# Optimization experiments

Hardware: AMD Instinct MI355X
Metric: run time of the kernel (lower is better)

The kernel has to match this reference:

```python
import jax, jax.numpy as jnp
import numpy as np

D_STATE = 8
DT_RANK = 16
D_CONV = 4


def layernorm(x, w, b, eps=1e-5):
    mu = jnp.mean(x, axis=-1, keepdims=True)
    var = jnp.var(x, axis=-1, keepdims=True)
    return (x - mu) * jax.lax.rsqrt(var + eps) * w + b


def silu(x):
    return x * jax.nn.sigmoid(x)


def dwconv_causal(x, w, b):
    # x: [B,L,D], w: [D,K] depthwise causal conv (mamba conv1d, padding=K-1 then truncate)
    K = w.shape[1]
    xp = jnp.pad(x, ((0, 0), (K - 1, 0), (0, 0)))
    y = jax.lax.conv_general_dilated(
        xp, w.T[:, None, :], (1,), 'VALID',
        dimension_numbers=('NWC', 'WIO', 'NWC'),
        feature_group_count=w.shape[0])
    return y + b


def selective_scan(u, dt, A, Bm, Cm, Dp):
    # u, dt: [b,l,d]; A: [d,n]; Bm, Cm: [b,l,n]; Dp: [d]
    def step(h, inp):
        dt_t, B_t, C_t, u_t = inp           # [b,d],[b,n],[b,n],[b,d]
        dA = jnp.exp(dt_t[..., None] * A)   # [b,d,n]
        h = dA * h + dt_t[..., None] * B_t[:, None, :] * u_t[..., None]
        y = jnp.einsum('bdn,bn->bd', h, C_t)
        return h, y
    b, l, d = u.shape
    h0 = jnp.zeros((b, d, A.shape[1]), u.dtype)
    xs = (dt.transpose(1, 0, 2), Bm.transpose(1, 0, 2),
          Cm.transpose(1, 0, 2), u.transpose(1, 0, 2))
    _, ys = jax.lax.scan(step, h0, xs)
    return ys.transpose(1, 0, 2) + u * Dp


def scan_dir(x, xe, cw, cb, cew, ceb, xpw, dtw, dtb, A_log, Dp):
    # one scan direction: u from x (input0 path), dt/B/C from xe (extra_emb path)
    xc = silu(dwconv_causal(x, cw, cb))
    ec = silu(dwconv_causal(xe, cew, ceb))
    dbl = ec @ xpw.T                                   # [b,l,dt_rank+2n]
    dtr = dbl[..., :DT_RANK]
    Bm = dbl[..., DT_RANK:DT_RANK + D_STATE]
    Cm = dbl[..., DT_RANK + D_STATE:]
    dt = jax.nn.softplus(dtr @ dtw.T + dtb)
    A = -jnp.exp(A_log)
    return selective_scan(xc, dt, A, Bm, Cm, Dp)


def forward(input0, input1, norm0_w, norm0_b, norm1_w, norm1_b,
            in_proj_w, in_proj_extra_w,
            convx_w, convx_b, conve_w, conve_b,
            convx_w_r, convx_b_r, conve_w_r, conve_b_r,
            xproj_w, xproj_w_r, dtproj_w, dtproj_b, dtproj_w_r, dtproj_b_r,
            A_log, A_log_r, Dp, Dp_r, outnorm_w, outnorm_b, outproj_w):
    skip = input0
    h0 = layernorm(input0, norm0_w, norm0_b)
    h1 = layernorm(input1, norm1_w, norm1_b)
    xz = h0 @ in_proj_w.T                     # [b,l,2d]
    d = in_proj_w.shape[0] // 2
    x, z = xz[..., :d], xz[..., d:]
    xe = h1 @ in_proj_extra_w.T               # [b,l,d]
    # forward-direction scan
    y_f = scan_dir(x, xe, convx_w, convx_b, conve_w, conve_b,
                   xproj_w, dtproj_w, dtproj_b, A_log, Dp)
    # backward-direction scan (flip sequence, scan, flip back)
    xr, xer = jnp.flip(x, 1), jnp.flip(xe, 1)
    y_b = scan_dir(xr, xer, convx_w_r, convx_b_r, conve_w_r, conve_b_r,
                   xproj_w_r, dtproj_w_r, dtproj_b_r, A_log_r, Dp_r)
    y = (y_f + jnp.flip(y_b, 1)) * 0.5        # if_devide_out=True
    y = layernorm(y, outnorm_w, outnorm_b)    # use_norm=True
    y = y * silu(z)
    out = y @ outproj_w.T
    return out + skip


def setup_inputs() -> dict:
    key = jax.random.key(0)
    B, H, W, dim = 2, 128, 128, 256
    L, d, n, dtr, K = H * W, dim, D_STATE, DT_RANK, D_CONV
    ks = jax.random.split(key, 24)
    s = 0.02
    inp = {
        'input0': jax.random.normal(ks[0], (B, L, dim), jnp.float32),
        'input1': jax.random.normal(ks[1], (B, L, dim), jnp.float32),
        'norm0_w': jnp.ones((dim,), jnp.float32),
        'norm0_b': jnp.zeros((dim,), jnp.float32),
        'norm1_w': jnp.ones((dim,), jnp.float32),
        'norm1_b': jnp.zeros((dim,), jnp.float32),
        'in_proj_w': jax.random.normal(ks[2], (2 * d, dim), jnp.float32) * s,
        'in_proj_extra_w': jax.random.normal(ks[3], (d, dim), jnp.float32) * s,
        'convx_w': jax.random.normal(ks[4], (d, K), jnp.float32) * 0.2,
        'convx_b': jnp.zeros((d,), jnp.float32),
        'conve_w': jax.random.normal(ks[5], (d, K), jnp.float32) * 0.2,
        'conve_b': jnp.zeros((d,), jnp.float32),
        'convx_w_r': jax.random.normal(ks[6], (d, K), jnp.float32) * 0.2,
        'convx_b_r': jnp.zeros((d,), jnp.float32),
        'conve_w_r': jax.random.normal(ks[7], (d, K), jnp.float32) * 0.2,
        'conve_b_r': jnp.zeros((d,), jnp.float32),
        'xproj_w': jax.random.normal(ks[8], (dtr + 2 * n, d), jnp.float32) * s,
        'xproj_w_r': jax.random.normal(ks[9], (dtr + 2 * n, d), jnp.float32) * s,
        'dtproj_w': jax.random.normal(ks[10], (d, dtr), jnp.float32) * 0.1,
        'dtproj_b': jax.random.uniform(ks[11], (d,), jnp.float32, -4.0, -2.0),
        'dtproj_w_r': jax.random.normal(ks[12], (d, dtr), jnp.float32) * 0.1,
        'dtproj_b_r': jax.random.uniform(ks[13], (d,), jnp.float32, -4.0, -2.0),
        'A_log': jnp.tile(jnp.log(jnp.arange(1, n + 1, dtype=jnp.float32)), (d, 1)),
        'A_log_r': jnp.tile(jnp.log(jnp.arange(1, n + 1, dtype=jnp.float32)), (d, 1)),
        'Dp': jnp.ones((d,), jnp.float32),
        'Dp_r': jnp.ones((d,), jnp.float32),
        'outnorm_w': jnp.ones((d,), jnp.float32),
        'outnorm_b': jnp.zeros((d,), jnp.float32),
        'outproj_w': jax.random.normal(ks[14], (dim, d), jnp.float32) * s,
    }
    return inp


def reference(input0, input1, norm0_w, norm0_b, norm1_w, norm1_b,
              in_proj_w, in_proj_extra_w,
              convx_w, convx_b, conve_w, conve_b,
              convx_w_r, convx_b_r, conve_w_r, conve_b_r,
              xproj_w, xproj_w_r, dtproj_w, dtproj_b, dtproj_w_r, dtproj_b_r,
              A_log, A_log_r, Dp, Dp_r, outnorm_w, outnorm_b, outproj_w):
    return forward(input0, input1, norm0_w, norm0_b, norm1_w, norm1_b,
                   in_proj_w, in_proj_extra_w,
                   convx_w, convx_b, conve_w, conve_b,
                   convx_w_r, convx_b_r, conve_w_r, conve_b_r,
                   xproj_w, xproj_w_r, dtproj_w, dtproj_b, dtproj_w_r, dtproj_b_r,
                   A_log, A_log_r, Dp, Dp_r, outnorm_w, outnorm_b, outproj_w)
```

## Files before the change

kernel.cpp:

```cpp
#include <hip/hip_runtime.h>
#include <math.h>

#define L_SEQ 16384
#define DIM 256
#define NST 8
#define RNK 16
#define S_TOT 32768
#define NCH 512
#define CLH 32

typedef __attribute__((ext_vector_type(8))) short bf16x8;
typedef __attribute__((ext_vector_type(4))) float f32x4;

__device__ __forceinline__ float bf2f(unsigned short u) {
  union { unsigned int i; float f; } v; v.i = ((unsigned int)u) << 16; return v.f;
}
__device__ __forceinline__ unsigned short f2bf(float x) {
  union { float f; unsigned int i; } v; v.f = x;
  unsigned int r = v.i + 0x7fffu + ((v.i >> 16) & 1u);
  return (unsigned short)(r >> 16);
}
__device__ __forceinline__ float rcpf(float x) {
  return __builtin_amdgcn_rcpf(x);
}

__global__ __launch_bounds__(256) void ln_norm(
    const float* __restrict__ in0, const float* __restrict__ in1,
    const float* __restrict__ w0, const float* __restrict__ b0,
    const float* __restrict__ w1, const float* __restrict__ b1,
    unsigned short* __restrict__ h0, unsigned short* __restrict__ h1,
    const float* __restrict__ pw0, const float* __restrict__ pw1,
    const float* __restrict__ pw2, unsigned short* __restrict__ wbout) {
  int which = blockIdx.y;
  if (which == 0 && blockIdx.x < 1024) {
    int i = blockIdx.x * 256 + threadIdx.x;
    if (i < 131072) wbout[i] = f2bf(pw0[i]);
    else if (i < 196608) wbout[i] = f2bf(pw1[i - 131072]);
    else wbout[i] = f2bf(pw2[i - 196608]);
  }
  int row = blockIdx.x * 4 + (threadIdx.x >> 6);
  int lane = threadIdx.x & 63;
  const float* x = (which ? in1 : in0) + (size_t)row * DIM;
  const float* w = which ? w1 : w0;
  const float* b = which ? b1 : b0;
  unsigned short* h = which ? h1 : h0;
  float4 v = *(const float4*)&x[lane * 4];
  float s = v.x + v.y + v.z + v.w;
  float s2 = v.x * v.x + v.y * v.y + v.z * v.z + v.w * v.w;
  for (int off = 32; off; off >>= 1) {
    s += __shfl_xor(s, off);
    s2 += __shfl_xor(s2, off);
  }
  float mean = s * (1.0f / DIM);
  float var = s2 * (1.0f / DIM) - mean * mean;
  float rstd = rsqrtf(var + 1e-5f);
  float4 wv = *(const float4*)&w[lane * 4];
  float4 bv = *(const float4*)&b[lane * 4];
  ushort4 out;
  out.x = f2bf((v.x - mean) * rstd * wv.x + bv.x);
  out.y = f2bf((v.y - mean) * rstd * wv.y + bv.y);
  out.z = f2bf((v.z - mean) * rstd * wv.z + bv.z);
  out.w = f2bf((v.w - mean) * rstd * wv.w + bv.w);
  *(ushort4*)&h[(size_t)row * DIM + lane * 4] = out;
}

template <int BF16C, int ADDIN>
__global__ __launch_bounds__(256) void gemm64(
    const unsigned short* __restrict__ A, int lda,
    const unsigned short* __restrict__ Wb,
    void* __restrict__ Cv, const float* __restrict__ addp, int Nn) {
  __shared__ unsigned short As[64 * 256];
  __shared__ unsigned short Ws[64 * 256];
  int tid = threadIdx.x;
  int n0 = blockIdx.x * 64, m0 = blockIdx.y * 64;
  for (int i = 0; i < 8; ++i) {
    int f8 = tid + i * 256;
    int r = f8 >> 5, c8 = (f8 & 31) * 8;
    int sc = c8 ^ ((r & 7) << 3);
    *(uint4*)&As[r * 256 + sc] = *(const uint4*)&A[(size_t)(m0 + r) * lda + c8];
    *(uint4*)&Ws[r * 256 + sc] = *(const uint4*)&Wb[(size_t)(n0 + r) * 256 + c8];
  }
  __syncthreads();
  int wid = tid >> 6, lane = tid & 63;
  int wm = wid >> 1, wn = wid & 1;
  int l15 = lane & 15, lk = (lane >> 4) * 8;
  f32x4 acc[2][2] = {};
  for (int ks = 0; ks < 8; ++ks) {
    int kcol = ks * 32 + lk;
    bf16x8 af[2], bf_[2];
    for (int mf = 0; mf < 2; ++mf) {
      int row = wm * 32 + mf * 16 + l15;
      af[mf] = *(const bf16x8*)&As[row * 256 + (kcol ^ ((row & 7) << 3))];
    }
    for (int nf = 0; nf < 2; ++nf) {
      int row = wn * 32 + nf * 16 + l15;
      bf_[nf] = *(const bf16x8*)&Ws[row * 256 + (kcol ^ ((row & 7) << 3))];
    }
    for (int mf = 0; mf < 2; ++mf)
      for (int nf = 0; nf < 2; ++nf)
        acc[mf][nf] = __builtin_amdgcn_mfma_f32_16x16x32_bf16(
            af[mf], bf_[nf], acc[mf][nf], 0, 0, 0);
  }
  for (int mf = 0; mf < 2; ++mf)
    for (int nf = 0; nf < 2; ++nf) {
      int row = m0 + wm * 32 + mf * 16 + (lane >> 4) * 4;
      int col = n0 + wn * 32 + nf * 16 + l15;
      for (int v = 0; v < 4; ++v) {
        size_t off = (size_t)(row + v) * Nn + col;
        float val = acc[mf][nf][v];
        if (ADDIN) val += addp[off];
        if (BF16C) ((unsigned short*)Cv)[off] = f2bf(val);
        else       ((float*)Cv)[off] = val;
      }
    }
}

__global__ __launch_bounds__(256) void xproj_mfma(
    const unsigned short* __restrict__ xe,
    const float* __restrict__ conve_w, const float* __restrict__ conve_b,
    const float* __restrict__ conve_w_r, const float* __restrict__ conve_b_r,
    const float* __restrict__ xproj_w, const float* __restrict__ xproj_w_r,
    unsigned short* __restrict__ dbl2) {
  __shared__ unsigned short ecS[64 * 256];
  __shared__ unsigned short xwS[32 * 256];
  int chunk = blockIdx.x;
  int dir = blockIdx.y;
  int b = chunk >> 8;
  int t0 = (chunk & 255) * 64;
  int tid = threadIdx.x;
  const float* cw = dir ? conve_w_r : conve_w;
  const float* cb = dir ? conve_b_r : conve_b;
  const float* xw = dir ? xproj_w_r : xproj_w;

  for (int i = tid; i < 32 * 256; i += 256) {
    int o = i >> 8, dd = i & 255;
    xwS[o * 256 + (((dd & ~7) ^ ((o & 7) << 3)) | (dd & 7))] = f2bf(xw[i]);
  }

  {
    int c = tid;
    float w0 = cw[c * 4 + 0], w1 = cw[c * 4 + 1], w2 = cw[c * 4 + 2],
          w3 = cw[c * 4 + 3], bias = cb[c];
    size_t bL = (size_t)b * L_SEQ;
    auto loadx = [&](int t) -> float {
      if (t < 0) return 0.f;
      int src = dir ? (L_SEQ - 1 - t) : t;
      return bf2f(xe[(bL + src) * DIM + c]);
    };
    float xm3 = loadx(t0 - 3), xm2 = loadx(t0 - 2), xm1 = loadx(t0 - 1);
    const unsigned short* xp =
        &xe[(bL + (dir ? (L_SEQ - 1 - t0) : t0)) * DIM + c];
    int xstep = dir ? -DIM : DIM;
    int cbase = c & ~7, clow = c & 7;
    for (int t4 = 0; t4 < 64; t4 += 4) {
      float xin4[4];
      for (int j = 0; j < 4; ++j) xin4[j] = bf2f(xp[(ptrdiff_t)j * xstep]);
      xp += (ptrdiff_t)4 * xstep;
      for (int j = 0; j < 4; ++j) {
        int tl = t4 + j;
        float xin = xin4[j];
        float pre = w0 * xm3 + w1 * xm2 + w2 * xm1 + w3 * xin + bias;
        float u = pre * rcpf(1.f + __expf(-pre));
        xm3 = xm2; xm2 = xm1; xm1 = xin;
        ecS[tl * 256 + ((cbase ^ ((tl & 7) << 3)) | clow)] = f2bf(u);
      }
    }
  }
  __syncthreads();

  int wid = tid >> 6, lane = tid & 63;
  int l15 = lane & 15, lk = (lane >> 4) * 8;
  f32x4 acc[2] = {};
  for (int kk = 0; kk < 8; ++kk) {
    int kcol = kk * 32 + lk;
    int row = wid * 16 + l15;
    bf16x8 af = *(const bf16x8*)&ecS[row * 256 + (kcol ^ ((row & 7) << 3))];
    for (int ni = 0; ni < 2; ++ni) {
      int o = ni * 16 + l15;
      bf16x8 bfr = *(const bf16x8*)&xwS[o * 256 + (kcol ^ ((o & 7) << 3))];
      acc[ni] = __builtin_amdgcn_mfma_f32_16x16x32_bf16(af, bfr, acc[ni], 0, 0, 0);
    }
  }
  size_t mbase = (size_t)dir * S_TOT + (size_t)chunk * 64;
  int rloc = wid * 16 + (lane >> 4) * 4;
  for (int ni = 0; ni < 2; ++ni) {
    int o = ni * 16 + l15;
    for (int v = 0; v < 4; ++v)
      dbl2[(mbase + rloc + v) * 32 + o] = f2bf(acc[ni][v]);
  }
}

__global__ __launch_bounds__(256) void dtu_compute(
    const unsigned short* __restrict__ dbl2,
    const float* __restrict__ dtw, const float* __restrict__ dtw_r,
    const float* __restrict__ dtb, const float* __restrict__ dtb_r,
    unsigned short* __restrict__ dt_arr,
    const unsigned short* __restrict__ xz,
    const float* __restrict__ convx_w, const float* __restrict__ convx_b,
    const float* __restrict__ convx_w_r, const float* __restrict__ convx_b_r,
    unsigned short* __restrict__ u_arr) {
  __shared__ unsigned short dtwS[256 * 32];
  __shared__ unsigned short dtrS[64 * 32];
  __shared__ unsigned short outS[64 * 256];
  int tid = threadIdx.x;
  if (blockIdx.x < 1024) {
    int m0 = blockIdx.x * 64;
    int dir = (blockIdx.x >= 512) ? 1 : 0;
    const float* dw = dir ? dtw_r : dtw;
    const float* db = dir ? dtb_r : dtb;
    {
      uint4 z; z.x = 0; z.y = 0; z.z = 0; z.w = 0;
      for (int i = tid; i < 1280; i += 256) {
        if (i < 1024) ((uint4*)dtwS)[i] = z;
        else          ((uint4*)dtrS)[i - 1024] = z;
      }
    }
    __syncthreads();
    for (int it = 0; it < 4; ++it) {
      int idx = tid + it * 256;
      int c = idx >> 2, k4 = idx & 3;
      float4 v = *(const float4*)&dw[c * 16 + k4 * 4];
      uint2 pk;
      pk.x = (unsigned int)f2bf(v.x) | ((unsigned int)f2bf(v.y) << 16);
      pk.y = (unsigned int)f2bf(v.z) | ((unsigned int)f2bf(v.w) << 16);
      int byte = c * 64 + (((k4 >> 1) ^ (c & 3)) << 4) + ((k4 & 1) << 3);
      *(uint2*)((char*)dtwS + byte) = pk;
    }
    {
      int r = tid >> 2, k4 = tid & 3;
      uint2 pk = *(const uint2*)&dbl2[(size_t)(m0 + r) * 32 + k4 * 4];
      int byte = r * 64 + (((k4 >> 1) ^ (r & 3)) << 4) + ((k4 & 1) << 3);
      *(uint2*)((char*)dtrS + byte) = pk;
    }
    __syncthreads();
    int wid = tid >> 6, lane = tid & 63;
    int l15 = lane & 15, lkc = lane >> 4;
    bf16x8 af[4];
    for (int mi = 0; mi < 4; ++mi) {
      int r = mi * 16 + l15;
      af[mi] = *(const bf16x8*)((char*)dtrS + r * 64 + ((lkc ^ (r & 3)) << 4));
    }
    f32x4 acc[4][4] = {};
    for (int ni = 0; ni < 4; ++ni) {
      int c = (wid * 4 + ni) * 16 + l15;
      bf16x8 bfr = *(const bf16x8*)((char*)dtwS + c * 64 + ((lkc ^ (c & 3)) << 4));
      for (int mi = 0; mi < 4; ++mi)
        acc[mi][ni] = __builtin_amdgcn_mfma_f32_16x16x32_bf16(
            af[mi], bfr, acc[mi][ni], 0, 0, 0);
    }
    for (int ni = 0; ni < 4; ++ni) {
      int c = (wid * 4 + ni) * 16 + l15;
      float bias_ = db[c];
      int cb_ = c & ~7, cl_ = c & 7;
      for (int mi = 0; mi < 4; ++mi) {
        int rb = mi * 16 + (lane >> 4) * 4;
        for (int v = 0; v < 4; ++v) {
          int r = rb + v;
          float xdt = acc[mi][ni][v] + bias_;
          float dtv = (xdt > 15.f) ? xdt : __logf(1.f + __expf(xdt));
          outS[r * 256 + ((cb_ ^ ((r & 7) << 3)) | cl_)] = f2bf(dtv);
        }
      }
    }
    __syncthreads();
    for (int it = 0; it < 8; ++it) {
      int i = tid + it * 256;
      int r = i >> 5, cg = (i & 31) * 8;
      uint4 val = *(const uint4*)&outS[r * 256 + (cg ^ ((r & 7) << 3))];
      *(uint4*)&dt_arr[(size_t)(m0 + r) * 256 + cg] = val;
    }
  } else {
    int chunk = blockIdx.x - 1024;
    int b = chunk >> 9;
    int t0 = (chunk & 511) * 32;
    int c = tid;
    float w0 = convx_w[c * 4 + 0], w1 = convx_w[c * 4 + 1],
          w2 = convx_w[c * 4 + 2], w3 = convx_w[c * 4 + 3], bias = convx_b[c];
    float w0r = convx_w_r[c * 4 + 0], w1r = convx_w_r[c * 4 + 1],
          w2r = convx_w_r[c * 4 + 2], w3r = convx_w_r[c * 4 + 3],
          biasr = convx_b_r[c];
    size_t bL = (size_t)b * L_SEQ;
    auto ld = [&](int t) -> float {
      if (t < 0 || t >= L_SEQ) return 0.f;
      return bf2f(xz[(bL + t) * 512 + c]);
    };
    float x3 = ld(t0 - 3), x2 = ld(t0 - 2), x1 = ld(t0 - 1);
    unsigned short* op0 = &u_arr[(bL + t0) * DIM + c];
    unsigned short* op1 =
        &u_arr[((size_t)S_TOT + bL + (L_SEQ - 1 - t0)) * DIM + c];
    for (int tg = 0; tg < 36; tg += 4) {
      float xin4[4];
      for (int j = 0; j < 4; ++j) xin4[j] = ld(t0 + tg + j);
      for (int j = 0; j < 4; ++j) {
        int tl = tg + j;
        float xin = xin4[j];
        if (tl < 32) {
          float pre = w0 * x3 + w1 * x2 + w2 * x1 + w3 * xin + bias;
          op0[(size_t)tl * DIM] = f2bf(pre * rcpf(1.f + __expf(-pre)));
        }
        if (tl >= 3 && tl < 35) {
          float prer = w0r * xin + w1r * x1 + w2r * x2 + w3r * x3 + biasr;
          int s = tl - 3;
          *(op1 - (ptrdiff_t)s * DIM) = f2bf(prer * rcpf(1.f + __expf(-prer)));
        }
        x3 = x2; x2 = x1; x1 = xin;
      }
    }
  }
}

#define DA8(FASTA)                                                    \
  float dA[NST];                                                      \
  if (FASTA) {                                                        \
    float e1 = __expf(-dtv);                                          \
    dA[0] = e1;                                                       \
    for (int n = 1; n < NST; ++n) dA[n] = dA[n - 1] * e1;             \
  } else {                                                            \
    for (int n = 0; n < NST; ++n) dA[n] = __expf(dtv * Ar[n]);        \
  }

template <int USE_UDT>
__global__ __launch_bounds__(256) void scan_pass1(
    const unsigned short* __restrict__ xz, const unsigned short* __restrict__ dbl2,
    const unsigned short* __restrict__ u_arr,
    const unsigned short* __restrict__ dt_arr,
    const float* __restrict__ convx_w, const float* __restrict__ convx_b,
    const float* __restrict__ convx_w_r, const float* __restrict__ convx_b_r,
    const float* __restrict__ dtproj_w, const float* __restrict__ dtproj_b,
    const float* __restrict__ dtproj_w_r, const float* __restrict__ dtproj_b_r,
    const float* __restrict__ A_log, const float* __restrict__ A_log_r,
    float* __restrict__ Pc, float* __restrict__ Qc) {
  int chunk = blockIdx.x, b = blockIdx.y, dir = blockIdx.z;
  int d = threadIdx.x;
  const float* al = dir ? A_log_r : A_log;
  float w0 = 0.f, w1 = 0.f, w2 = 0.f, w3 = 0.f, bias = 0.f, dbias = 0.f;
  float dwreg[RNK];
  if (!USE_UDT) {
    const float* cw = dir ? convx_w_r : convx_w;
    const float* cb = dir ? convx_b_r : convx_b;
    const float* dw = dir ? dtproj_w_r : dtproj_w;
    const float* dbp = dir ? dtproj_b_r : dtproj_b;
    w0 = cw[d * 4 + 0]; w1 = cw[d * 4 + 1]; w2 = cw[d * 4 + 2];
    w3 = cw[d * 4 + 3]; bias = cb[d]; dbias = dbp[d];
    for (int r = 0; r < RNK; ++r) dwreg[r] = dw[d * RNK + r];
  }
  float Ar[NST];
  bool fa = true;
  for (int n = 0; n < NST; ++n) {
    Ar[n] = -__expf(al[d * NST + n]);
    fa = fa && (fabsf(Ar[n] + (float)(n + 1)) < 1e-4f * (float)(n + 1));
  }
  bool fastA = (__ballot(fa) == ~0ULL);

  __shared__ float dblS[CLH][32];
  int t0 = chunk * CLH;
  size_t dtbase = (size_t)dir * S_TOT + (size_t)b * L_SEQ;
  if (USE_UDT) {
    int i = d;
    dblS[i >> 3][i & 7] =
        bf2f(dbl2[(dtbase + t0 + (i >> 3)) * 32 + 16 + (i & 7)]);
  } else {
    for (int i = d; i < CLH * 32; i += 256)
      dblS[i >> 5][i & 31] = bf2f(dbl2[(dtbase + t0) * 32 + i]);
  }
  __syncthreads();
  auto loadx = [&](int t) -> float {
    if (t < 0) return 0.f;
    int srct = dir ? (L_SEQ - 1 - t) : t;
    return bf2f(xz[((size_t)b * L_SEQ + srct) * 512 + d]);
  };
  float xm3 = 0.f, xm2 = 0.f, xm1 = 0.f;
  if (!USE_UDT) { xm3 = loadx(t0 - 3); xm2 = loadx(t0 - 2); xm1 = loadx(t0 - 1); }
  const unsigned short* up = &u_arr[(dtbase + t0) * DIM + d];
  const unsigned short* dtp = &dt_arr[(dtbase + t0) * DIM + d];
  float Q[NST];
  for (int n = 0; n < NST; ++n) Q[n] = 0.f;
  float sdt = 0.f;
  const int BOFF = USE_UDT ? 0 : 16;

#define P1_GRP(FASTA)                                                      \
  for (int t8 = 0; t8 < CLH; t8 += 8) {                                    \
    float uu[8], dd[8];                                                    \
    for (int j = 0; j < 8; ++j) {                                          \
      uu[j] = bf2f(up[(size_t)j * DIM]);                                   \
      dd[j] = bf2f(dtp[(size_t)j * DIM]);                                  \
    }                                                                      \
    up += 8 * DIM; dtp += 8 * DIM;                                         \
    for (int j = 0; j < 8; ++j) {                                          \
      const float* row = dblS[t8 + j];                                     \
      float u = uu[j], dtv = dd[j];                                        \
      float du = dtv * u;                                                  \
      sdt += dtv;                                                          \
      DA8(FASTA)                                                           \
      float4 B0 = *(const float4*)(row);                                   \
      float4 B1 = *(const float4*)(row + 4);                               \
      Q[0] = dA[0] * Q[0] + du * B0.x; Q[1] = dA[1] * Q[1] + du * B0.y;    \
      Q[2] = dA[2] * Q[2] + du * B0.z; Q[3] = dA[3] * Q[3] + du * B0.w;    \
      Q[4] = dA[4] * Q[4] + du * B1.x; Q[5] = dA[5] * Q[5] + du * B1.y;    \
      Q[6] = dA[6] * Q[6] + du * B1.z; Q[7] = dA[7] * Q[7] + du * B1.w;    \
    }                                                                      \
  }

#define P1_STEP(FASTA)                                                     \
  {                                                                        \
    const float* row = dblS[tl];                                           \
    float u, dtv;                                                          \
    {                                                                      \
      float xin = loadx(t0 + tl);                                          \
      float pre = w0 * xm3 + w1 * xm2 + w2 * xm1 + w3 * xin + bias;        \
      u = pre * rcpf(1.f + __expf(-pre));                                  \
      xm3 = xm2; xm2 = xm1; xm1 = xin;                                     \
      float4 q0 = *(const float4*)(row);                                   \
      float4 q1 = *(const float4*)(row + 4);                               \
      float4 q2 = *(const float4*)(row + 8);                               \
      float4 q3 = *(const float4*)(row + 12);                              \
      float xdt = dbias + q0.x * dwreg[0] + q0.y * dwreg[1] +              \
                  q0.z * dwreg[2] + q0.w * dwreg[3] + q1.x * dwreg[4] +    \
                  q1.y * dwreg[5] + q1.z * dwreg[6] + q1.w * dwreg[7] +    \
                  q2.x * dwreg[8] + q2.y * dwreg[9] + q2.z * dwreg[10] +   \
                  q2.w * dwreg[11] + q3.x * dwreg[12] + q3.y * dwreg[13] + \
                  q3.z * dwreg[14] + q3.w * dwreg[15];                     \
      dtv = (xdt > 15.f) ? xdt : __logf(1.f + __expf(xdt));                \
    }                                                                      \
    float du = dtv * u;                                                    \
    sdt += dtv;                                                            \
    DA8(FASTA)                                                             \
    float4 B0 = *(const float4*)(row + BOFF);                              \
    float4 B1 = *(const float4*)(row + BOFF + 4);                          \
    Q[0] = dA[0] * Q[0] + du * B0.x; Q[1] = dA[1] * Q[1] + du * B0.y;      \
    Q[2] = dA[2] * Q[2] + du * B0.z; Q[3] = dA[3] * Q[3] + du * B0.w;      \
    Q[4] = dA[4] * Q[4] + du * B1.x; Q[5] = dA[5] * Q[5] + du * B1.y;      \
    Q[6] = dA[6] * Q[6] + du * B1.z; Q[7] = dA[7] * Q[7] + du * B1.w;      \
  }

  if (USE_UDT) {
    if (fastA) { P1_GRP(1) } else { P1_GRP(0) }
  } else {
    if (fastA) {
      for (int tl = 0; tl < CLH; ++tl) P1_STEP(1)
    } else {
      for (int tl = 0; tl < CLH; ++tl) P1_STEP(0)
    }
  }
#undef P1_STEP
#undef P1_GRP

  float P[NST];
  if (fastA) {
    float E = __expf(-sdt);
    P[0] = E;
    for (int n = 1; n < NST; ++n) P[n] = P[n - 1] * E;
  } else {
    for (int n = 0; n < NST; ++n) P[n] = __expf(Ar[n] * sdt);
  }
  size_t obase = ((((size_t)(dir * 2 + b)) * NCH + chunk) * DIM + d) * NST;
  for (int n = 0; n < NST; ++n) { Pc[obase + n] = P[n]; Qc[obase + n] = Q[n]; }
}

__global__ __launch_bounds__(256) void scan_mid(
    float* __restrict__ Pc, const float* __restrict__ Qc) {
  int idx = blockIdx.x * 256 + threadIdx.x;
  int dn = idx & 2047;
  int db_ = idx >> 11;
  size_t base = (size_t)db_ * NCH * 2048 + dn;
  float h = 0.f;
  for (int c0 = 0; c0 < NCH; c0 += 8) {
    size_t off = base + (size_t)c0 * 2048;
    float P[8], Q[8];
#pragma unroll
    for (int j = 0; j < 8; ++j) {
      P[j] = Pc[off + (size_t)j * 2048];
      Q[j] = Qc[off + (size_t)j * 2048];
    }
#pragma unroll
    for (int j = 0; j < 8; ++j) {
      Pc[off + (size_t)j * 2048] = h;
      h = P[j] * h + Q[j];
    }
  }
}

template <int MODE>
__global__ __launch_bounds__(256) void scan_pass2(
    const unsigned short* __restrict__ xz, const unsigned short* __restrict__ dbl2,
    unsigned short* __restrict__ u_arr,
    const unsigned short* __restrict__ dt_arr,
    const float* __restrict__ convx_w, const float* __restrict__ convx_b,
    const float* __restrict__ convx_w_r, const float* __restrict__ convx_b_r,
    const float* __restrict__ dtproj_w, const float* __restrict__ dtproj_b,
    const float* __restrict__ dtproj_w_r, const float* __restrict__ dtproj_b_r,
    const float* __restrict__ A_log, const float* __restrict__ A_log_r,
    const float* __restrict__ Dp, const float* __restrict__ Dp_r,
    const float* __restrict__ Hinit, unsigned short* __restrict__ ycomb,
    int dirParam) {
  int chunk = blockIdx.x, b = blockIdx.y;
  int dir = MODE ? blockIdx.z : dirParam;
  int d = threadIdx.x;
  const float* al = dir ? A_log_r : A_log;
  float Dv = (dir ? Dp_r : Dp)[d];
  float w0 = 0.f, w1 = 0.f, w2 = 0.f, w3 = 0.f, bias = 0.f, dbias = 0.f;
  float dwreg[RNK];
  if (!MODE) {
    const float* cw = dir ? convx_w_r : convx_w;
    const float* cb = dir ? convx_b_r : convx_b;
    const float* dw = dir ? dtproj_w_r : dtproj_w;
    const float* dbp = dir ? dtproj_b_r : dtproj_b;
    w0 = cw[d * 4 + 0]; w1 = cw[d * 4 + 1]; w2 = cw[d * 4 + 2];
    w3 = cw[d * 4 + 3]; bias = cb[d];
    dbias = dbp[d];
    for (int r = 0; r < RNK; ++r) dwreg[r] = dw[d * RNK + r];
  }
  float Ar[NST];
  bool fa = true;
  for (int n = 0; n < NST; ++n) {
    Ar[n] = -__expf(al[d * NST + n]);
    fa = fa && (fabsf(Ar[n] + (float)(n + 1)) < 1e-4f * (float)(n + 1));
  }
  bool fastA = (__ballot(fa) == ~0ULL);

  __shared__ float dblS[CLH][32];
  int t0 = chunk * CLH;
  size_t dtbase = (size_t)dir * S_TOT + (size_t)b * L_SEQ;
  if (MODE) {
    for (int i = d; i < CLH * 16; i += 256)
      dblS[i >> 4][i & 15] =
          bf2f(dbl2[(dtbase + t0 + (i >> 4)) * 32 + 16 + (i & 15)]);
  } else {
    for (int i = d; i < CLH * 32; i += 256)
      dblS[i >> 5][i & 31] = bf2f(dbl2[(dtbase + t0) * 32 + i]);
  }
  __syncthreads();
  auto loadx = [&](int t) -> float {
    if (t < 0) return 0.f;
    int srct = dir ? (L_SEQ - 1 - t) : t;
    return bf2f(xz[((size_t)b * L_SEQ + srct) * 512 + d]);
  };
  float xm3 = 0.f, xm2 = 0.f, xm1 = 0.f;
  if (!MODE) { xm3 = loadx(t0 - 3); xm2 = loadx(t0 - 2); xm1 = loadx(t0 - 1); }
  float h[NST];
  size_t hbase = ((((size_t)(dir * 2 + b)) * NCH + chunk) * DIM + d) * NST;
  for (int n = 0; n < NST; ++n) h[n] = Hinit[hbase + n];
  unsigned short* up = &u_arr[(dtbase + t0) * DIM + d];
  const unsigned short* dtp = &dt_arr[(dtbase + t0) * DIM + d];
  unsigned short* yc = &ycomb[((size_t)b * L_SEQ + t0) * DIM + d];

#define P2_GRP(FASTA)                                                      \
  for (int t8 = 0; t8 < CLH; t8 += 8) {                                    \
    float uu[8], dd[8];                                                    \
    for (int j = 0; j < 8; ++j) {                                          \
      uu[j] = bf2f(up[(size_t)j * DIM]);                                   \
      dd[j] = bf2f(dtp[(size_t)j * DIM]);                                  \
    }                                                                      \
    for (int j = 0; j < 8; ++j) {                                          \
      const float* row = dblS[t8 + j];                                     \
      float u = uu[j], dtv = dd[j];                                        \
      float du = dtv * u;                                                  \
      DA8(FASTA)                                                           \
      float4 B0 = *(const float4*)(row);                                   \
      float4 B1 = *(const float4*)(row + 4);                               \
      float4 C0 = *(const float4*)(row + 8);                               \
      float4 C1 = *(const float4*)(row + 12);                              \
      h[0] = dA[0] * h[0] + du * B0.x; h[1] = dA[1] * h[1] + du * B0.y;    \
      h[2] = dA[2] * h[2] + du * B0.z; h[3] = dA[3] * h[3] + du * B0.w;    \
      h[4] = dA[4] * h[4] + du * B1.x; h[5] = dA[5] * h[5] + du * B1.y;    \
      h[6] = dA[6] * h[6] + du * B1.z; h[7] = dA[7] * h[7] + du * B1.w;    \
      float y = C0.x * h[0] + C0.y * h[1] + C0.z * h[2] + C0.w * h[3] +    \
                C1.x * h[4] + C1.y * h[5] + C1.z * h[6] + C1.w * h[7] +    \
                u * Dv;                                                    \
      if (dir == 0) yc[(size_t)j * DIM] = f2bf(y);                         \
      else          up[(size_t)j * DIM] = f2bf(y);                         \
    }                                                                      \
    up += 8 * DIM; dtp += 8 * DIM; yc += 8 * DIM;                          \
  }

#define P2_STEP(FASTA)                                                     \
  {                                                                        \
    int t = t0 + tl;                                                       \
    const float* row = dblS[tl];                                           \
    float u, dtv;                                                          \
    {                                                                      \
      float xin = loadx(t);                                                \
      float pre = w0 * xm3 + w1 * xm2 + w2 * xm1 + w3 * xin + bias;        \
      u = pre * rcpf(1.f + __expf(-pre));                                  \
      xm3 = xm2; xm2 = xm1; xm1 = xin;                                     \
      float4 q0 = *(const float4*)(row);                                   \
      float4 q1 = *(const float4*)(row + 4);                               \
      float4 q2 = *(const float4*)(row + 8);                               \
      float4 q3 = *(const float4*)(row + 12);                              \
      float xdt = dbias + q0.x * dwreg[0] + q0.y * dwreg[1] +              \
                  q0.z * dwreg[2] + q0.w * dwreg[3] + q1.x * dwreg[4] +    \
                  q1.y * dwreg[5] + q1.z * dwreg[6] + q1.w * dwreg[7] +    \
                  q2.x * dwreg[8] + q2.y * dwreg[9] + q2.z * dwreg[10] +   \
                  q2.w * dwreg[11] + q3.x * dwreg[12] + q3.y * dwreg[13] + \
                  q3.z * dwreg[14] + q3.w * dwreg[15];                     \
      dtv = (xdt > 15.f) ? xdt : __logf(1.f + __expf(xdt));                \
    }                                                                      \
    float du = dtv * u;                                                    \
    DA8(FASTA)                                                             \
    float4 B0 = *(const float4*)(row + 16);                                \
    float4 B1 = *(const float4*)(row + 20);                                \
    float4 C0 = *(const float4*)(row + 24);                                \
    float4 C1 = *(const float4*)(row + 28);                                \
    h[0] = dA[0] * h[0] + du * B0.x; h[1] = dA[1] * h[1] + du * B0.y;      \
    h[2] = dA[2] * h[2] + du * B0.z; h[3] = dA[3] * h[3] + du * B0.w;      \
    h[4] = dA[4] * h[4] + du * B1.x; h[5] = dA[5] * h[5] + du * B1.y;      \
    h[6] = dA[6] * h[6] + du * B1.z; h[7] = dA[7] * h[7] + du * B1.w;      \
    float y = C0.x * h[0] + C0.y * h[1] + C0.z * h[2] + C0.w * h[3] +      \
              C1.x * h[4] + C1.y * h[5] + C1.z * h[6] + C1.w * h[7] +      \
              u * Dv;                                                      \
    if (dir == 0) {                                                        \
      ycomb[((size_t)b * L_SEQ + t) * DIM + d] = f2bf(y);                  \
    } else {                                                               \
      size_t o = ((size_t)b * L_SEQ + (L_SEQ - 1 - t)) * DIM + d;          \
      float prev = bf2f(ycomb[o]);                                         \
      ycomb[o] = f2bf(0.5f * (prev + y));                                  \
    }                                                                      \
  }

  if (MODE) {
    if (fastA) { P2_GRP(1) } else { P2_GRP(0) }
  } else {
    if (fastA) {
      for (int tl = 0; tl < CLH; ++tl) P2_STEP(1)
    } else {
      for (int tl = 0; tl < CLH; ++tl) P2_STEP(0)
    }
  }
#undef P2_STEP
#undef P2_GRP
}

template <int MERGED>
__global__ __launch_bounds__(256) void combine_ln(
    const unsigned short* __restrict__ ycomb,
    const unsigned short* __restrict__ ybu,
    unsigned short* __restrict__ xz,
    const float* __restrict__ onw, const float* __restrict__ onb) {
  int m = blockIdx.x * 4 + (threadIdx.x >> 6);
  int lane = threadIdx.x & 63;
  ushort4 y4 = *(const ushort4*)&ycomb[(size_t)m * DIM + lane * 4];
  float v0 = bf2f(y4.x), v1 = bf2f(y4.y), v2 = bf2f(y4.z), v3 = bf2f(y4.w);
  if (MERGED) {
    int b = m >> 14, l = m & (L_SEQ - 1);
    size_t fo = ((size_t)S_TOT + (size_t)b * L_SEQ + (L_SEQ - 1 - l)) * DIM +
                lane * 4;
    ushort4 yb4 = *(const ushort4*)&ybu[fo];
    v0 = 0.5f * (v0 + bf2f(yb4.x)); v1 = 0.5f * (v1 + bf2f(yb4.y));
    v2 = 0.5f * (v2 + bf2f(yb4.z)); v3 = 0.5f * (v3 + bf2f(yb4.w));
  }
  float s = v0 + v1 + v2 + v3;
  float s2 = v0 * v0 + v1 * v1 + v2 * v2 + v3 * v3;
  for (int off = 32; off; off >>= 1) {
    s += __shfl_xor(s, off);
    s2 += __shfl_xor(s2, off);
  }
  float mean = s * (1.0f / DIM);
  float var = s2 * (1.0f / DIM) - mean * mean;
  float rstd = rsqrtf(var + 1e-5f);
  ushort4 z4 = *(const ushort4*)&xz[(size_t)m * 512 + 256 + lane * 4];
  float zf[4] = {bf2f(z4.x), bf2f(z4.y), bf2f(z4.z), bf2f(z4.w)};
  float vf[4] = {v0, v1, v2, v3};
  ushort4 out;
  unsigned short* op = (unsigned short*)&out;
  for (int j = 0; j < 4; ++j) {
    int c = lane * 4 + j;
    float ln = (vf[j] - mean) * rstd * onw[c] + onb[c];
    op[j] = f2bf(ln * (zf[j] * rcpf(1.f + __expf(-zf[j]))));
  }
  *(ushort4*)&xz[(size_t)m * 512 + lane * 4] = out;
}

extern "C" void kernel_launch(void* const* d_in, const int* in_sizes, int n_in,
                              void* d_out, int out_size, void* d_ws, size_t ws_size,
                              hipStream_t stream) {
  const float* input0 = (const float*)d_in[0];
  const float* input1 = (const float*)d_in[1];
  const float* norm0_w = (const float*)d_in[2];
  const float* norm0_b = (const float*)d_in[3];
  const float* norm1_w = (const float*)d_in[4];
  const float* norm1_b = (const float*)d_in[5];
  const float* in_proj_w = (const float*)d_in[6];
  const float* in_proj_extra_w = (const float*)d_in[7];
  const float* convx_w = (const float*)d_in[8];
  const float* convx_b = (const float*)d_in[9];
  const float* conve_w = (const float*)d_in[10];
  const float* conve_b = (const float*)d_in[11];
  const float* convx_w_r = (const float*)d_in[12];
  const float* convx_b_r = (const float*)d_in[13];
  const float* conve_w_r = (const float*)d_in[14];
  const float* conve_b_r = (const float*)d_in[15];
  const float* xproj_w = (const float*)d_in[16];
  const float* xproj_w_r = (const float*)d_in[17];
  const float* dtproj_w = (const float*)d_in[18];
  const float* dtproj_b = (const float*)d_in[19];
  const float* dtproj_w_r = (const float*)d_in[20];
  const float* dtproj_b_r = (const float*)d_in[21];
  const float* A_log = (const float*)d_in[22];
  const float* A_log_r = (const float*)d_in[23];
  const float* Dp = (const float*)d_in[24];
  const float* Dp_r = (const float*)d_in[25];
  const float* outnorm_w = (const float*)d_in[26];
  const float* outnorm_b = (const float*)d_in[27];
  const float* outproj_w = (const float*)d_in[28];

  char* w = (char*)d_ws;
  unsigned short* xz    = (unsigned short*)(w + 0);
  unsigned short* h1    = (unsigned short*)(w + 0);
  unsigned short* h0    = (unsigned short*)(w + 33554432);
  unsigned short* ycomb = (unsigned short*)(w + 33554432);
  float* Qc   = (float*)(w + 33554432);
  unsigned short* xe    = (unsigned short*)(w + 50331648);
  float* Pc   = (float*)(w + 50331648);
  unsigned short* dbl2 = (unsigned short*)(w + 67108864);
  unsigned short* wb = (unsigned short*)(w + 75497472);
  unsigned short* wb_in  = wb;
  unsigned short* wb_ex  = wb + 131072;
  unsigned short* wb_out = wb + 196608;
  unsigned short* u_arr  = (unsigned short*)(w + 76021760);
  unsigned short* dt_arr = (unsigned short*)(w + 109576192);
  const bool big = ws_size >= 76021760ULL + 67108864ULL;

  ln_norm<<<dim3(S_TOT / 4, 2), 256, 0, stream>>>(
      input0, input1, norm0_w, norm0_b, norm1_w, norm1_b, h0, h1,
      in_proj_w, in_proj_extra_w, outproj_w, wb);
  gemm64<1, 0><<<dim3(4, 512), 256, 0, stream>>>(h1, DIM, wb_ex, xe, nullptr, 256);
  gemm64<1, 0><<<dim3(8, 512), 256, 0, stream>>>(h0, DIM, wb_in, xz, nullptr, 512);
  xproj_mfma<<<dim3(512, 2), 256, 0, stream>>>(
      xe, conve_w, conve_b, conve_w_r, conve_b_r, xproj_w, xproj_w_r, dbl2);
  if (big) {
    dtu_compute<<<dim3(2048), 256, 0, stream>>>(
        dbl2, dtproj_w, dtproj_w_r, dtproj_b, dtproj_b_r, dt_arr,
        xz, convx_w, convx_b, convx_w_r, convx_b_r, u_arr);
    scan_pass1<1><<<dim3(NCH, 2, 2), 256, 0, stream>>>(
        xz, dbl2, u_arr, dt_arr, convx_w, convx_b, convx_w_r, convx_b_r,
        dtproj_w, dtproj_b, dtproj_w_r, dtproj_b_r, A_log, A_log_r, Pc, Qc);
  } else {
    scan_pass1<0><<<dim3(NCH, 2, 2), 256, 0, stream>>>(
        xz, dbl2, u_arr, dt_arr, convx_w, convx_b, convx_w_r, convx_b_r,
        dtproj_w, dtproj_b, dtproj_w_r, dtproj_b_r, A_log, A_log_r, Pc, Qc);
  }
  scan_mid<<<dim3(32), 256, 0, stream>>>(Pc, Qc);
  if (big) {
    scan_pass2<1><<<dim3(NCH, 2, 2), 256, 0, stream>>>(
        xz, dbl2, u_arr, dt_arr, convx_w, convx_b, convx_w_r, convx_b_r,
        dtproj_w, dtproj_b, dtproj_w_r, dtproj_b_r, A_log, A_log_r,
        Dp, Dp_r, Pc, ycomb, 0);
    combine_ln<1><<<dim3(S_TOT / 4), 256, 0, stream>>>(
        ycomb, u_arr, xz, outnorm_w, outnorm_b);
  } else {
    for (int dir = 0; dir < 2; ++dir)
      scan_pass2<0><<<dim3(NCH, 2), 256, 0, stream>>>(
          xz, dbl2, u_arr, dt_arr, convx_w, convx_b, convx_w_r, convx_b_r,
          dtproj_w, dtproj_b, dtproj_w_r, dtproj_b_r, A_log, A_log_r,
          Dp, Dp_r, Pc, ycomb, dir);
    combine_ln<0><<<dim3(S_TOT / 4), 256, 0, stream>>>(
        ycomb, nullptr, xz, outnorm_w, outnorm_b);
  }
  gemm64<0, 1><<<dim3(4, 512), 256, 0, stream>>>(
      xz, 512, wb_out, d_out, input0, 256);
}
```

Measured before the change: 219.0 us.

## Merge input GEMMs into one launch and fuse combine+layernorm+gate into output GEMM

The two input projection GEMMs now run as one grid that selects its operand by block index, with h1 moved to a separate buffer so both can run together. The forward/backward combine, output layernorm and SiLU gate are folded into the A-tile load of the output projection GEMM. This removes a launch and the bf16 round trip of the gated activations through xz, at the cost of redoing the layernorm per N-tile (4x redundant loads and math) and more LDS traffic.

Measured after the change: 237.8 us. +8.6%, slower.

```diff
diff --git a/kernel.cpp b/kernel.cpp
--- a/kernel.cpp
+++ b/kernel.cpp
@@ -111,6 +111,182 @@
         if (ADDIN) val += addp[off];
         if (BF16C) ((unsigned short*)Cv)[off] = f2bf(val);
         else       ((float*)Cv)[off] = val;
+      }
+    }
+}
+
+__global__ __launch_bounds__(256) void gemm_in(
+    const unsigned short* __restrict__ h0, const unsigned short* __restrict__ h1,
+    const unsigned short* __restrict__ wb_in, const unsigned short* __restrict__ wb_ex,
+    unsigned short* __restrict__ xzOut, unsigned short* __restrict__ xeOut) {
+  __shared__ unsigned short As[64 * 256];
+  __shared__ unsigned short Ws[64 * 256];
+  int tid = threadIdx.x;
+  bool isX = blockIdx.x >= 4;
+  const unsigned short* A = isX ? h0 : h1;
+  const unsigned short* Wb = isX ? wb_in : wb_ex;
+  unsigned short* Cv = isX ? xzOut : xeOut;
+  int Nn = isX ? 512 : 256;
+  int n0 = (isX ? (int)blockIdx.x - 4 : (int)blockIdx.x) * 64;
+  int m0 = blockIdx.y * 64;
+  for (int i = 0; i < 8; ++i) {
+    int f8 = tid + i * 256;
+    int r = f8 >> 5, c8 = (f8 & 31) * 8;
+    int sc = c8 ^ ((r & 7) << 3);
+    *(uint4*)&As[r * 256 + sc] = *(const uint4*)&A[(size_t)(m0 + r) * 256 + c8];
+    *(uint4*)&Ws[r * 256 + sc] = *(const uint4*)&Wb[(size_t)(n0 + r) * 256 + c8];
+  }
+  __syncthreads();
+  int wid = tid >> 6, lane = tid & 63;
+  int wm = wid >> 1, wn = wid & 1;
+  int l15 = lane & 15, lk = (lane >> 4) * 8;
+  f32x4 acc[2][2] = {};
+  for (int ks = 0; ks < 8; ++ks) {
+    int kcol = ks * 32 + lk;
+    bf16x8 af[2], bf_[2];
+    for (int mf = 0; mf < 2; ++mf) {
+      int row = wm * 32 + mf * 16 + l15;
+      af[mf] = *(const bf16x8*)&As[row * 256 + (kcol ^ ((row & 7) << 3))];
+    }
+    for (int nf = 0; nf < 2; ++nf) {
+      int row = wn * 32 + nf * 16 + l15;
+      bf_[nf] = *(const bf16x8*)&Ws[row * 256 + (kcol ^ ((row & 7) << 3))];
+    }
+    for (int mf = 0; mf < 2; ++mf)
+      for (int nf = 0; nf < 2; ++nf)
+        acc[mf][nf] = __builtin_amdgcn_mfma_f32_16x16x32_bf16(
+            af[mf], bf_[nf], acc[mf][nf], 0, 0, 0);
+  }
+  for (int mf = 0; mf < 2; ++mf)
+    for (int nf = 0; nf < 2; ++nf) {
+      int row = m0 + wm * 32 + mf * 16 + (lane >> 4) * 4;
+      int col = n0 + wn * 32 + nf * 16 + l15;
+      for (int v = 0; v < 4; ++v) {
+        size_t off = (size_t)(row + v) * Nn + col;
+        Cv[off] = f2bf(acc[mf][nf][v]);
+      }
+    }
+}
+
+__global__ __launch_bounds__(256) void gemm_out_fused(
+    const unsigned short* __restrict__ ycomb,
+    const unsigned short* __restrict__ ybu,
+    const unsigned short* __restrict__ xz,
+    const float* __restrict__ onw, const float* __restrict__ onb,
+    const unsigned short* __restrict__ Wb,
+    float* __restrict__ outp, const float* __restrict__ addp) {
+  __shared__ unsigned short As[64 * 256];
+  __shared__ unsigned short Ws[64 * 256];
+  __shared__ float muS[64], rsS[64];
+  int tid = threadIdx.x;
+  int n0 = blockIdx.x * 64, m0 = blockIdx.y * 64;
+  for (int i = 0; i < 8; ++i) {
+    int f8 = tid + i * 256;
+    int r = f8 >> 5, c8 = (f8 & 31) * 8;
+    int sc = c8 ^ ((r & 7) << 3);
+    *(uint4*)&Ws[r * 256 + sc] = *(const uint4*)&Wb[(size_t)(n0 + r) * 256 + c8];
+    int m = m0 + r;
+    int b = m >> 14, l = m & (L_SEQ - 1);
+    const unsigned short* pf = &ycomb[(size_t)m * DIM + c8];
+    const unsigned short* pb =
+        &ybu[((size_t)S_TOT + ((size_t)b << 14) + (L_SEQ - 1 - l)) * DIM + c8];
+    ushort4 f0 = *(const ushort4*)pf, f1 = *(const ushort4*)(pf + 4);
+    ushort4 b0 = *(const ushort4*)pb, b1 = *(const ushort4*)(pb + 4);
+    float v[8];
+    v[0] = 0.5f * (bf2f(f0.x) + bf2f(b0.x));
+    v[1] = 0.5f * (bf2f(f0.y) + bf2f(b0.y));
+    v[2] = 0.5f * (bf2f(f0.z) + bf2f(b0.z));
+    v[3] = 0.5f * (bf2f(f0.w) + bf2f(b0.w));
+    v[4] = 0.5f * (bf2f(f1.x) + bf2f(b1.x));
+    v[5] = 0.5f * (bf2f(f1.y) + bf2f(b1.y));
+    v[6] = 0.5f * (bf2f(f1.z) + bf2f(b1.z));
+    v[7] = 0.5f * (bf2f(f1.w) + bf2f(b1.w));
+    float s = 0.f, s2 = 0.f;
+    for (int j = 0; j < 8; ++j) { s += v[j]; s2 += v[j] * v[j]; }
+    for (int off = 16; off; off >>= 1) {
+      s += __shfl_xor(s, off);
+      s2 += __shfl_xor(s2, off);
+    }
+    if ((tid & 31) == 0) {
+      float mean = s * (1.0f / DIM);
+      float var = s2 * (1.0f / DIM) - mean * mean;
+      muS[r] = mean;
+      rsS[r] = rsqrtf(var + 1e-5f);
+    }
+    uint4 pk;
+    pk.x = (unsigned int)f2bf(v[0]) | ((unsigned int)f2bf(v[1]) << 16);
+    pk.y = (unsigned int)f2bf(v[2]) | ((unsigned int)f2bf(v[3]) << 16);
+    pk.z = (unsigned int)f2bf(v[4]) | ((unsigned int)f2bf(v[5]) << 16);
+    pk.w = (unsigned int)f2bf(v[6]) | ((unsigned int)f2bf(v[7]) << 16);
+    *(uint4*)&As[r * 256 + sc] = pk;
+  }
+  __syncthreads();
+  for (int i = 0; i < 8; ++i) {
+    int f8 = tid + i * 256;
+    int r = f8 >> 5, c8 = (f8 & 31) * 8;
+    int sc = c8 ^ ((r & 7) << 3);
+    int m = m0 + r;
+    uint4 pk = *(const uint4*)&As[r * 256 + sc];
+    float v[8];
+    v[0] = bf2f((unsigned short)(pk.x & 0xffff));
+    v[1] = bf2f((unsigned short)(pk.x >> 16));
+    v[2] = bf2f((unsigned short)(pk.y & 0xffff));
+    v[3] = bf2f((unsigned short)(pk.y >> 16));
+    v[4] = bf2f((unsigned short)(pk.z & 0xffff));
+    v[5] = bf2f((unsigned short)(pk.z >> 16));
+    v[6] = bf2f((unsigned short)(pk.w & 0xffff));
+    v[7] = bf2f((unsigned short)(pk.w >> 16));
+    const unsigned short* pz = &xz[(size_t)m * 512 + 256 + c8];
+    ushort4 z0 = *(const ushort4*)pz, z1 = *(const ushort4*)(pz + 4);
+    float zf[8] = {bf2f(z0.x), bf2f(z0.y), bf2f(z0.z), bf2f(z0.w),
+                   bf2f(z1.x), bf2f(z1.y), bf2f(z1.z), bf2f(z1.w)};
+    float4 w0 = *(const float4*)&onw[c8];
+    float4 w1 = *(const float4*)&onw[c8 + 4];
+    float4 bb0 = *(const float4*)&onb[c8];
+    float4 bb1 = *(const float4*)&onb[c8 + 4];
+    float wv[8] = {w0.x, w0.y, w0.z, w0.w, w1.x, w1.y, w1.z, w1.w};
+    float bv[8] = {bb0.x, bb0.y, bb0.z, bb0.w, bb1.x, bb1.y, bb1.z, bb1.w};
+    float mean = muS[r], rstd = rsS[r];
+    unsigned int o[4];
+    for (int jj = 0; jj < 4; ++jj) {
+      int j0 = jj * 2, j1 = jj * 2 + 1;
+      float ln0 = (v[j0] - mean) * rstd * wv[j0] + bv[j0];
+      float ln1 = (v[j1] - mean) * rstd * wv[j1] + bv[j1];
+      float g0 = ln0 * (zf[j0] * rcpf(1.f + __expf(-zf[j0])));
+      float g1 = ln1 * (zf[j1] * rcpf(1.f + __expf(-zf[j1])));
+      o[jj] = (unsigned int)f2bf(g0) | ((unsigned int)f2bf(g1) << 16);
+    }
+    uint4 w4; w4.x = o[0]; w4.y = o[1]; w4.z = o[2]; w4.w = o[3];
+    *(uint4*)&As[r * 256 + sc] = w4;
+  }
+  __syncthreads();
+  int wid = tid >> 6, lane = tid & 63;
+  int wm = wid >> 1, wn = wid & 1;
+  int l15 = lane & 15, lk = (lane >> 4) * 8;
+  f32x4 acc[2][2] = {};
+  for (int ks = 0; ks < 8; ++ks) {
+    int kcol = ks * 32 + lk;
+    bf16x8 af[2], bf_[2];
+    for (int mf = 0; mf < 2; ++mf) {
+      int row = wm * 32 + mf * 16 + l15;
+      af[mf] = *(const bf16x8*)&As[row * 256 + (kcol ^ ((row & 7) << 3))];
+    }
+    for (int nf = 0; nf < 2; ++nf) {
+      int row = wn * 32 + nf * 16 + l15;
+      bf_[nf] = *(const bf16x8*)&Ws[row * 256 + (kcol ^ ((row & 7) << 3))];
+    }
+    for (int mf = 0; mf < 2; ++mf)
+      for (int nf = 0; nf < 2; ++nf)
+        acc[mf][nf] = __builtin_amdgcn_mfma_f32_16x16x32_bf16(
+            af[mf], bf_[nf], acc[mf][nf], 0, 0, 0);
+  }
+  for (int mf = 0; mf < 2; ++mf)
+    for (int nf = 0; nf < 2; ++nf) {
+      int row = m0 + wm * 32 + mf * 16 + (lane >> 4) * 4;
+      int col = n0 + wn * 32 + nf * 16 + l15;
+      for (int v = 0; v < 4; ++v) {
+        size_t off = (size_t)(row + v) * 256 + col;
+        outp[off] = acc[mf][nf][v] + addp[off];
       }
     }
 }
@@ -630,24 +806,14 @@
 #undef P2_GRP
 }
 
-template <int MERGED>
 __global__ __launch_bounds__(256) void combine_ln(
     const unsigned short* __restrict__ ycomb,
-    const unsigned short* __restrict__ ybu,
     unsigned short* __restrict__ xz,
     const float* __restrict__ onw, const float* __restrict__ onb) {
   int m = blockIdx.x * 4 + (threadIdx.x >> 6);
   int lane = threadIdx.x & 63;
   ushort4 y4 = *(const ushort4*)&ycomb[(size_t)m * DIM + lane * 4];
   float v0 = bf2f(y4.x), v1 = bf2f(y4.y), v2 = bf2f(y4.z), v3 = bf2f(y4.w);
-  if (MERGED) {
-    int b = m >> 14, l = m & (L_SEQ - 1);
-    size_t fo = ((size_t)S_TOT + (size_t)b * L_SEQ + (L_SEQ - 1 - l)) * DIM +
-                lane * 4;
-    ushort4 yb4 = *(const ushort4*)&ybu[fo];
-    v0 = 0.5f * (v0 + bf2f(yb4.x)); v1 = 0.5f * (v1 + bf2f(yb4.y));
-    v2 = 0.5f * (v2 + bf2f(yb4.z)); v3 = 0.5f * (v3 + bf2f(yb4.w));
-  }
   float s = v0 + v1 + v2 + v3;
   float s2 = v0 * v0 + v1 * v1 + v2 * v2 + v3 * v3;
   for (int off = 32; off; off >>= 1) {
@@ -705,7 +871,6 @@
 
   char* w = (char*)d_ws;
   unsigned short* xz    = (unsigned short*)(w + 0);
-  unsigned short* h1    = (unsigned short*)(w + 0);
   unsigned short* h0    = (unsigned short*)(w + 33554432);
   unsigned short* ycomb = (unsigned short*)(w + 33554432);
   float* Qc   = (float*)(w + 33554432);
@@ -719,12 +884,17 @@
   unsigned short* u_arr  = (unsigned short*)(w + 76021760);
   unsigned short* dt_arr = (unsigned short*)(w + 109576192);
   const bool big = ws_size >= 76021760ULL + 67108864ULL;
+  unsigned short* h1 = big ? u_arr : xz;
 
   ln_norm<<<dim3(S_TOT / 4, 2), 256, 0, stream>>>(
       input0, input1, norm0_w, norm0_b, norm1_w, norm1_b, h0, h1,
       in_proj_w, in_proj_extra_w, outproj_w, wb);
-  gemm64<1, 0><<<dim3(4, 512), 256, 0, stream>>>(h1, DIM, wb_ex, xe, nullptr, 256);
-  gemm64<1, 0><<<dim3(8, 512), 256, 0, stream>>>(h0, DIM, wb_in, xz, nullptr, 512);
+  if (big) {
+    gemm_in<<<dim3(12, 512), 256, 0, stream>>>(h0, h1, wb_in, wb_ex, xz, xe);
+  } else {
+    gemm64<1, 0><<<dim3(4, 512), 256, 0, stream>>>(h1, DIM, wb_ex, xe, nullptr, 256);
+    gemm64<1, 0><<<dim3(8, 512), 256, 0, stream>>>(h0, DIM, wb_in, xz, nullptr, 512);
+  }
   xproj_mfma<<<dim3(512, 2), 256, 0, stream>>>(
       xe, conve_w, conve_b, conve_w_r, conve_b_r, xproj_w, xproj_w_r, dbl2);
   if (big) {
@@ -745,17 +915,16 @@
         xz, dbl2, u_arr, dt_arr, convx_w, convx_b, convx_w_r, convx_b_r,
         dtproj_w, dtproj_b, dtproj_w_r, dtproj_b_r, A_log, A_log_r,
         Dp, Dp_r, Pc, ycomb, 0);
-    combine_ln<1><<<dim3(S_TOT / 4), 256, 0, stream>>>(
-        ycomb, u_arr, xz, outnorm_w, outnorm_b);
+    gemm_out_fused<<<dim3(4, 512), 256, 0, stream>>>(
+        ycomb, u_arr, xz, outnorm_w, outnorm_b, wb_out, (float*)d_out, input0);
   } else {
     for (int dir = 0; dir < 2; ++dir)
       scan_pass2<0><<<dim3(NCH, 2), 256, 0, stream>>>(
           xz, dbl2, u_arr, dt_arr, convx_w, convx_b, convx_w_r, convx_b_r,
           dtproj_w, dtproj_b, dtproj_w_r, dtproj_b_r, A_log, A_log_r,
           Dp, Dp_r, Pc, ycomb, dir);
-    combine_ln<0><<<dim3(S_TOT / 4), 256, 0, stream>>>(
-        ycomb, nullptr, xz, outnorm_w, outnorm_b);
-  }
-  gemm64<0, 1><<<dim3(4, 512), 256, 0, stream>>>(
-      xz, 512, wb_out, d_out, input0, 256);
-}
+    combine_ln<<<dim3(S_TOT / 4), 256, 0, stream>>>(ycomb, xz, outnorm_w, outnorm_b);
+    gemm64<0, 1><<<dim3(4, 512), 256, 0, stream>>>(
+        xz, 512, wb_out, d_out, input0, 256);
+  }
+}
```
